# Optimization experiments

Hardware: AMD Instinct MI355X
Metric: run time of the kernel (lower is better)

The kernel has to match this reference:

```python
import math
import jax, jax.numpy as jnp
from jax import lax
import numpy as np

N, C, H, W = 32, 256, 56, 56

def setup_inputs() -> dict:
    key = jax.random.key(0)
    k = jax.random.split(key, 5)
    return {
        "x": jax.random.normal(k[0], (N, C, H, W), dtype=jnp.float32),
        "p1_w": jax.random.normal(k[1], (H, W, C, 1), dtype=jnp.float32) * 0.1,
        "conv_w": jax.random.normal(k[2], (C, C // 2, 3, 3), dtype=jnp.float32) * 0.05,
        "p4_w": jax.random.normal(k[3], (1, C, C), dtype=jnp.float32) * 0.1,
        "p5_w": jax.random.normal(k[4], (C, 1), dtype=jnp.float32) * 0.1,
    }

def reference(x, p1_w, conv_w, p4_w, p5_w):
    n, c, h, w = x.shape
    inv_sqrt_c = 1.0 / math.sqrt(c)
    # t_1: einsum 'abcd,cdef->abef' -> [n, c, c, 1] -> [n, c, c]
    t1 = jnp.einsum('nchw,hwef->ncef', x, p1_w)[..., 0]
    # t_3: grouped 3x3 conv, groups=2, no bias -> [n, c, h, w]
    t3 = lax.conv_general_dilated(
        x, conv_w, window_strides=(1, 1), padding=((1, 1), (1, 1)),
        dimension_numbers=('NCHW', 'OIHW', 'NCHW'), feature_group_count=2)
    # t_4: broadcast elementwise scale [1,c,c] * [n,c,c]
    t4 = p4_w * t1
    # t_5: [n,c,c] @ [c,1] -> [n,c]
    t5 = jnp.einsum('nab,bo->nao', t4, p5_w)[..., 0]
    # t_6: bmm(t4 [n,c,c], t3 [n,c,hw]) / sqrt(c) -> [n,c,h,w]
    t6 = (jnp.einsum('nab,nbs->nas', t4, t3.reshape(n, c, h * w))
          .reshape(n, c, h, w)) * inv_sqrt_c
    # t_7: bmm(t5 [n,1,c], x [n,c,hw]) / sqrt(c) -> [n,h,w]
    t7 = (jnp.einsum('nc,ncs->ns', t5, x.reshape(n, c, h * w))
          .reshape(n, h, w)) * inv_sqrt_c
    # t_8: broadcast add [n,1,h,w] + [n,c,h,w]
    return t7[:, None, :, :] + t6
```

## Files before the change

### kernel.cpp

```cpp
#include <hip/hip_runtime.h>

#define HWB   3136
#define HWPAD 3200
#define SPAD  3364

typedef __attribute__((ext_vector_type(8))) short bf16x8;
typedef __attribute__((ext_vector_type(4))) float f32x4;

__device__ __forceinline__ unsigned short f2bf(float f) {
    unsigned u = __float_as_uint(f);
    unsigned r = (u + 0x7fffu + ((u >> 16) & 1u)) >> 16;
    return (unsigned short)r;
}
__device__ __forceinline__ float bf2f(unsigned short h) {
    return __uint_as_float(((unsigned)h) << 16);
}
__device__ __forceinline__ void gl_lds16(const void* g, void* l) {
    __builtin_amdgcn_global_load_lds(
        (const __attribute__((address_space(1))) void*)g,
        (__attribute__((address_space(3))) void*)l, 16, 0, 0);
}

__global__ __launch_bounds__(256) void k_prep(
    const float* __restrict__ x, unsigned short* __restrict__ xc,
    unsigned short* __restrict__ xp)
{
    __shared__ short tile[64 * 66];
    const int n = blockIdx.z, c0 = blockIdx.y * 64, s0 = blockIdx.x * 64;
    const int t = threadIdx.x;
    const int cl = t >> 2;
    const int sq = (t & 3) * 16;

    const float* src = x + ((size_t)(n * 256 + c0 + cl)) * HWB + s0 + sq;
    unsigned short bf[16];
#pragma unroll
    for (int j = 0; j < 4; ++j) {
        float4 v = *(const float4*)(src + j * 4);
        bf[j * 4 + 0] = f2bf(v.x); bf[j * 4 + 1] = f2bf(v.y);
        bf[j * 4 + 2] = f2bf(v.z); bf[j * 4 + 3] = f2bf(v.w);
    }
    unsigned short* xcb = xc + ((size_t)(n * 256 + c0 + cl)) * HWB + s0 + sq;
    *(bf16x8*)xcb = *(const bf16x8*)&bf[0];
    *(bf16x8*)(xcb + 8) = *(const bf16x8*)&bf[8];
#pragma unroll
    for (int k = 0; k < 16; ++k)
        tile[(sq + k) * 66 + cl] = (short)bf[k];
    __syncthreads();
    const int r = t >> 2;
    const int cq = (t & 3) * 16;
    unsigned short ob[16];
#pragma unroll
    for (int j = 0; j < 8; ++j) {
        unsigned w = *(const unsigned*)&tile[r * 66 + cq + 2 * j];
        ob[2 * j] = (unsigned short)w;
        ob[2 * j + 1] = (unsigned short)(w >> 16);
    }
    const int s = s0 + r;
    const int sp = s + 2 * (s / 56) + 59;
    unsigned short* dst = xp + ((size_t)n * SPAD + sp) * 256 + c0 + cq;
    *(bf16x8*)dst = *(const bf16x8*)&ob[0];
    *(bf16x8*)(dst + 8) = *(const bf16x8*)&ob[8];
}

__global__ __launch_bounds__(256) void k_misc(
    const float* __restrict__ p1, const float* __restrict__ cw,
    unsigned short* __restrict__ p1t, unsigned short* __restrict__ wp,
    unsigned short* __restrict__ xp)
{
    const int b = blockIdx.x, t = threadIdx.x;
    if (b < 784) {
        __shared__ unsigned short tile[32][33];
        const int h0 = (b % 98) * 32, e0 = (b / 98) * 32;
        const int lx = t & 31, ly = t >> 5;
#pragma unroll
        for (int it = 0; it < 4; ++it) {
            int lh = ly + it * 8;
            tile[lh][lx] = f2bf(p1[(size_t)(h0 + lh) * 256 + e0 + lx]);
        }
        __syncthreads();
#pragma unroll
        for (int it = 0; it < 4; ++it) {
            int le = ly + it * 8;
            p1t[(size_t)(e0 + le) * HWB + h0 + lx] = tile[lx][le];
        }
    } else if (b < 1040) {
        const int o = b - 784;
#pragma unroll
        for (int k = t; k < 1152; k += 256) {
            int tap = k >> 7, ci = k & 127;
            wp[(size_t)o * 1152 + k] = f2bf(cw[(size_t)o * 1152 + ci * 9 + tap]);
        }
    } else {
        const int bb = b - 1040;
        const int n = bb / 29, xb = bb - n * 29;
        const int idx = xb * 256 + t;
        if (idx < 228 * 32) {
            const int i = idx >> 5, ch = idx & 31;
            int sp;
            if (i < 58)       sp = i;
            else if (i < 116) sp = 3306 + (i - 58);
            else if (i < 172) sp = (i - 115) * 58;
            else              sp = (i - 171) * 58 + 57;
            bf16x8 z = {};
            *(bf16x8*)&xp[((size_t)n * SPAD + sp) * 256 + ch * 8] = z;
        }
    }
}

__global__ __launch_bounds__(256) void k_conv(
    const unsigned short* __restrict__ xp, const unsigned short* __restrict__ wp,
    unsigned short* __restrict__ t3cl)
{
    __shared__ short As[2][128 * 64];
    __shared__ short Bs[2][128 * 64];
    const int tid = threadIdx.x;
    const int orig = blockIdx.x;
    const int wgid = (orig & 7) * 200 + (orig >> 3);
    const int ng = wgid / 25;
    const int tileS = (wgid - ng * 25) * 128;
    const int n = ng >> 1, g = ng & 1;
    const int wave = tid >> 6, lane = tid & 63;
    const int wm = (wave >> 1) * 64, wn = (wave & 1) * 64;

    const int rl = tid >> 3, q = tid & 7;
    const int swq = (q ^ (rl & 7)) * 8;

    const unsigned short* xpn = xp + (size_t)n * SPAD * 256 + g * 128 + swq;
    const unsigned short* arow[4];
    const unsigned short* brow[4];
#pragma unroll
    for (int p = 0; p < 4; ++p) {
        int s = tileS + p * 32 + rl;
        int sc = s < HWB ? s : HWB - 1;
        int sp = sc + 2 * (sc / 56) + 59;
        arow[p] = xpn + (size_t)sp * 256;
        brow[p] = wp + (size_t)(g * 128 + p * 32 + rl) * 1152 + swq;
    }

    f32x4 acc[4][4] = {};
    const int frow = lane & 15, quad = lane >> 4, sw = frow & 7;
    int rofA[4], rofB[4];
#pragma unroll
    for (int i = 0; i < 4; ++i) {
        rofA[i] = (wm + i * 16 + frow) * 64;
        rofB[i] = (wn + i * 16 + frow) * 64;
    }
    const int ldst = (tid >> 3) * 64 + (tid & 7) * 8;

    {
        const int shift0 = (-59) * 256;
#pragma unroll
        for (int p = 0; p < 4; ++p) {
            gl_lds16(arow[p] + shift0, &As[0][p * 2048 + ldst]);
            gl_lds16(brow[p], &Bs[0][p * 2048 + ldst]);
        }
    }
    __syncthreads();

    int cur = 0;
#pragma unroll
    for (int t = 0; t < 18; ++t) {
        if (t < 17) {
            const int tn = t + 1;
            const int tap = tn >> 1;
            const int shift = ((tap / 3 - 1) * 58 + (tap % 3 - 1)) * 256 + (tn & 1) * 64;
#pragma unroll
            for (int p = 0; p < 4; ++p) {
                gl_lds16(arow[p] + shift, &As[cur ^ 1][p * 2048 + ldst]);
                gl_lds16(brow[p] + tn * 64, &Bs[cur ^ 1][p * 2048 + ldst]);
            }
        }
        const short* Ab = As[cur];
        const short* Bb = Bs[cur];
#pragma unroll
        for (int h = 0; h < 2; ++h) {
            bf16x8 af[4], bfr[4];
#pragma unroll
            for (int i = 0; i < 4; ++i)
                af[i] = *(const bf16x8*)&Ab[rofA[i] + ((h * 4 + quad) ^ sw) * 8];
#pragma unroll
            for (int j = 0; j < 4; ++j)
                bfr[j] = *(const bf16x8*)&Bb[rofB[j] + ((h * 4 + quad) ^ sw) * 8];
#pragma unroll
            for (int i = 0; i < 4; ++i)
#pragma unroll
                for (int j = 0; j < 4; ++j)
                    acc[i][j] = __builtin_amdgcn_mfma_f32_16x16x32_bf16(af[i], bfr[j], acc[i][j], 0, 0, 0);
        }
        __syncthreads();
        cur ^= 1;
    }
    unsigned short* ob = t3cl + (size_t)n * HWPAD * 256 + g * 128;
#pragma unroll
    for (int i = 0; i < 4; ++i)
#pragma unroll
        for (int r = 0; r < 4; ++r) {
            int s = tileS + wm + i * 16 + (lane >> 4) * 4 + r;
            int c = wn + (lane & 15);
#pragma unroll
            for (int j = 0; j < 4; ++j) {
                float v = (s < HWB) ? acc[i][j][r] : 0.f;
                ob[(size_t)s * 256 + c + j * 16] = f2bf(v);
            }
        }
}

__global__ __launch_bounds__(256) void k_gemm1(
    const unsigned short* __restrict__ xc, const unsigned short* __restrict__ p1t,
    float* __restrict__ part)
{
    __shared__ short As[2][128 * 64];
    __shared__ short Bs[2][128 * 64];
    const int tid = threadIdx.x;
    const int orig = blockIdx.x;
    const int wgid = (orig & 7) * 64 + (orig >> 3);
    const int z = wgid >> 7;
    const int rem = wgid & 127;
    const int tileM = (rem >> 1) * 128;
    const int tileN = (rem & 1) * 128;
    const int kbase = z ? (832 + (z - 1) * 768) : 0;
    const int nk = z ? 12 : 13;
    const int wave = tid >> 6, lane = tid & 63;
    const int wm = (wave >> 1) * 64, wn = (wave & 1) * 64;

    const int rl = tid >> 3, q = tid & 7;
    const int swq = (q ^ (rl & 7)) * 8;
    const unsigned short* asrc = xc + (size_t)(tileM + rl) * HWB + kbase + swq;
    const unsigned short* bsrc = p1t + (size_t)(tileN + rl) * HWB + kbase + swq;

    f32x4 acc[4][4] = {};
    const int frow = lane & 15, quad = lane >> 4, sw = frow & 7;
    const int ldst = rl * 64 + q * 8;

#pragma unroll
    for (int p = 0; p < 4; ++p) {
        gl_lds16(asrc + (size_t)(p * 32) * HWB, &As[0][p * 2048 + ldst]);
        gl_lds16(bsrc + (size_t)(p * 32) * HWB, &Bs[0][p * 2048 + ldst]);
    }
    __syncthreads();

    int cur = 0;
    for (int i2 = 0; i2 < nk; ++i2) {
        if (i2 + 1 < nk) {
            const int kn = (i2 + 1) * 64;
#pragma unroll
            for (int p = 0; p < 4; ++p) {
                gl_lds16(asrc + (size_t)(p * 32) * HWB + kn, &As[cur ^ 1][p * 2048 + ldst]);
                gl_lds16(bsrc + (size_t)(p * 32) * HWB + kn, &Bs[cur ^ 1][p * 2048 + ldst]);
            }
        }
        const short* Ab = As[cur];
        const short* Bb = Bs[cur];
#pragma unroll
        for (int h = 0; h < 2; ++h) {
            bf16x8 af[4], bfr[4];
#pragma unroll
            for (int i = 0; i < 4; ++i)
                af[i] = *(const bf16x8*)&Ab[(wm + i * 16 + frow) * 64 + ((h * 4 + quad) ^ sw) * 8];
#pragma unroll
            for (int j = 0; j < 4; ++j)
                bfr[j] = *(const bf16x8*)&Bb[(wn + j * 16 + frow) * 64 + ((h * 4 + quad) ^ sw) * 8];
#pragma unroll
            for (int i = 0; i < 4; ++i)
#pragma unroll
                for (int j = 0; j < 4; ++j)
                    acc[i][j] = __builtin_amdgcn_mfma_f32_16x16x32_bf16(af[i], bfr[j], acc[i][j], 0, 0, 0);
        }
        __syncthreads();
        cur ^= 1;
    }
    float* ob = part + (size_t)z * 8192 * 256;
#pragma unroll
    for (int j = 0; j < 4; ++j) {
        const int e = tileN + wn + j * 16 + (lane & 15);
#pragma unroll
        for (int i = 0; i < 4; ++i)
#pragma unroll
            for (int r = 0; r < 4; ++r) {
                int m = tileM + wm + i * 16 + (lane >> 4) * 4 + r;
                ob[(size_t)m * 256 + e] = acc[i][j][r];
            }
    }
}

__global__ __launch_bounds__(256) void k_t4scale(
    const float* __restrict__ part, const float* __restrict__ p4,
    const float* __restrict__ p5, unsigned short* __restrict__ t4h,
    float* __restrict__ t5)
{
    const int row = blockIdx.x * 4 + (threadIdx.x >> 6);
    const int lane = threadIdx.x & 63;
    const size_t off = (size_t)row * 256 + lane * 4;
    const size_t slab = (size_t)8192 * 256;
    float4 a0 = *(const float4*)&part[off];
    float4 a1 = *(const float4*)&part[off + slab];
    float4 a2 = *(const float4*)&part[off + 2 * slab];
    float4 a3 = *(const float4*)&part[off + 3 * slab];
    float4 a;
    a.x = (a0.x + a1.x) + (a2.x + a3.x);
    a.y = (a0.y + a1.y) + (a2.y + a3.y);
    a.z = (a0.z + a1.z) + (a2.z + a3.z);
    a.w = (a0.w + a1.w) + (a2.w + a3.w);
    float4 sc = *(const float4*)&p4[(size_t)(row & 255) * 256 + lane * 4];
    float4 pv = *(const float4*)&p5[lane * 4];
    float v0 = a.x * sc.x, v1 = a.y * sc.y, v2 = a.z * sc.z, v3 = a.w * sc.w;
    ushort4 o;
    o.x = f2bf(v0); o.y = f2bf(v1); o.z = f2bf(v2); o.w = f2bf(v3);
    *(ushort4*)&t4h[(size_t)row * 256 + lane * 4] = o;
    float sum = v0 * pv.x + v1 * pv.y + v2 * pv.z + v3 * pv.w;
#pragma unroll
    for (int offd = 32; offd > 0; offd >>= 1) sum += __shfl_down(sum, offd);
    if (lane == 0) t5[row] = sum;
}

__global__ __launch_bounds__(256) void k_bmm(
    const unsigned short* __restrict__ t4h, const unsigned short* __restrict__ t3cl,
    const unsigned short* __restrict__ xp, const float* __restrict__ t5,
    float* __restrict__ out)
{
    __shared__ short As[2][128 * 64];
    __shared__ short Bs[2][128 * 64];
    __shared__ float t5s[256];
    __shared__ float t7loc[128];
    const int tid = threadIdx.x;
    const int orig = blockIdx.x;
    const int wgid = (orig & 7) * 200 + (orig >> 3);
    const int n = wgid / 50;
    const int rem = wgid - n * 50;
    const int tileA = (rem / 25) * 128;
    const int tileS = (rem % 25) * 128;
    const int wave = tid >> 6, lane = tid & 63;
    const int wm = (wave >> 1) * 64, wn = (wave & 1) * 64;

    const int rl = tid >> 3, q = tid & 7;
    const int swq = (q ^ (rl & 7)) * 8;
    const unsigned short* asrc = t4h + ((size_t)n * 256 + tileA + rl) * 256 + swq;
    const unsigned short* bsrc = t3cl + ((size_t)n * HWPAD + tileS + rl) * 256 + swq;

    f32x4 acc[4][4] = {};
    const int frow = lane & 15, quad = lane >> 4, sw = frow & 7;
    const int ldst = rl * 64 + q * 8;

    t5s[tid] = t5[n * 256 + tid];
#pragma unroll
    for (int p = 0; p < 4; ++p) {
        gl_lds16(asrc + (size_t)(p * 32) * 256, &As[0][p * 2048 + ldst]);
        gl_lds16(bsrc + (size_t)(p * 32) * 256, &Bs[0][p * 2048 + ldst]);
    }
    __syncthreads();

    if (tid < 128) {
        const int s = tileS + tid;
        float accv = 0.f;
        if (s < HWB) {
            const int sp = s + 2 * (s / 56) + 59;
            const unsigned short* row = xp + ((size_t)n * SPAD + sp) * 256;
#pragma unroll
            for (int j = 0; j < 32; ++j) {
                bf16x8 v = *(const bf16x8*)(row + j * 8);
#pragma unroll
                for (int k = 0; k < 8; ++k)
                    accv += t5s[j * 8 + k] * bf2f((unsigned short)v[k]);
            }
        }
        t7loc[tid] = accv * 0.0625f;
    }

    int cur = 0;
#pragma unroll
    for (int k0 = 0; k0 < 256; k0 += 64) {
        if (k0 < 192) {
            const int kn = k0 + 64;
#pragma unroll
            for (int p = 0; p < 4; ++p) {
                gl_lds16(asrc + (size_t)(p * 32) * 256 + kn, &As[cur ^ 1][p * 2048 + ldst]);
                gl_lds16(bsrc + (size_t)(p * 32) * 256 + kn, &Bs[cur ^ 1][p * 2048 + ldst]);
            }
        }
        const short* Ab = As[cur];
        const short* Bb = Bs[cur];
#pragma unroll
        for (int h = 0; h < 2; ++h) {
            bf16x8 af[4], bfr[4];
#pragma unroll
            for (int i = 0; i < 4; ++i)
                af[i] = *(const bf16x8*)&Ab[(wm + i * 16 + frow) * 64 + ((h * 4 + quad) ^ sw) * 8];
#pragma unroll
            for (int j = 0; j < 4; ++j)
                bfr[j] = *(const bf16x8*)&Bb[(wn + j * 16 + frow) * 64 + ((h * 4 + quad) ^ sw) * 8];
#pragma unroll
            for (int i = 0; i < 4; ++i)
#pragma unroll
                for (int j = 0; j < 4; ++j)
                    acc[i][j] = __builtin_amdgcn_mfma_f32_16x16x32_bf16(af[i], bfr[j], acc[i][j], 0, 0, 0);
        }
        __syncthreads();
        cur ^= 1;
    }
    float* ob = out + (size_t)n * 256 * HWB;
#pragma unroll
    for (int j = 0; j < 4; ++j) {
        const int sLoc = wn + j * 16 + (lane & 15);
        const int s = tileS + sLoc;
        if (s >= HWB) continue;
        const float t7v = t7loc[sLoc];
#pragma unroll
        for (int i = 0; i < 4; ++i)
#pragma unroll
            for (int r = 0; r < 4; ++r) {
                int a = tileA + wm + i * 16 + (lane >> 4) * 4 + r;
                ob[(size_t)a * HWB + s] = acc[i][j][r] * 0.0625f + t7v;
            }
    }
}

extern "C" void kernel_launch(void* const* d_in, const int* in_sizes, int n_in,
                              void* d_out, int out_size, void* d_ws, size_t ws_size,
                              hipStream_t stream) {
    const float* x  = (const float*)d_in[0];
    const float* p1 = (const float*)d_in[1];
    const float* cw = (const float*)d_in[2];
    const float* p4 = (const float*)d_in[3];
    const float* p5 = (const float*)d_in[4];

    char* w = (char*)d_ws;
    unsigned short* xp    = (unsigned short*)w;  w += (size_t)32 * SPAD * 256 * 2;
    unsigned short* t3cl  = (unsigned short*)w;  w += (size_t)32 * HWPAD * 256 * 2;
    unsigned short* p1t   = (unsigned short*)w;  w += (size_t)256 * HWB * 2;
    unsigned short* wpack = (unsigned short*)w;  w += (size_t)256 * 1152 * 2;
    unsigned short* t4h   = (unsigned short*)w;  w += (size_t)8192 * 256 * 2;
    float* t5             = (float*)w;           w += (size_t)8192 * 4;

    char* o = (char*)d_out;
    unsigned short* xc = (unsigned short*)o;
    float* part        = (float*)(o + (size_t)32 * 256 * HWB * 2);
    float* out = (float*)d_out;

    k_misc    <<<dim3(1968),      256, 0, stream>>>(p1, cw, p1t, wpack, xp);
    k_prep    <<<dim3(49, 4, 32), 256, 0, stream>>>(x, xc, xp);
    k_conv    <<<dim3(1600),      256, 0, stream>>>(xp, wpack, t3cl);
    k_gemm1   <<<dim3(512),       256, 0, stream>>>(xc, p1t, part);
    k_t4scale <<<dim3(2048),      256, 0, stream>>>(part, p4, p5, t4h, t5);
    k_bmm     <<<dim3(1600),      256, 0, stream>>>(t4h, t3cl, xp, t5, out);
}
```

Before: 344.6 us.

## Merge prep/misc kernels and conv/gemm1 into combined launches, halve split-K

Folds the x-conversion/transposition into the misc prep kernel and puts the grouped conv GEMM and the t1 GEMM into a single launch that branches on block index. The aim is to cut launch count and tail idle time by letting the two independent GEMMs share the GPU concurrently. The t1 GEMM split-K drops from 4 to 2 partial slabs with longer K loops, so the reduction reads less. The prep transposition now packs two channels per 32-bit LDS word. The trade-off is longer-running gemm1 blocks that may become the tail, and fewer blocks for that GEMM.

```diff
diff --git a/kernel.cpp b/kernel.cpp
--- a/kernel.cpp
+++ b/kernel.cpp
@@ -23,54 +23,52 @@
 
 __global__ __launch_bounds__(256) void k_prep(
     const float* __restrict__ x, unsigned short* __restrict__ xc,
-    unsigned short* __restrict__ xp)
-{
-    __shared__ short tile[64 * 66];
-    const int n = blockIdx.z, c0 = blockIdx.y * 64, s0 = blockIdx.x * 64;
-    const int t = threadIdx.x;
-    const int cl = t >> 2;
-    const int sq = (t & 3) * 16;
-
-    const float* src = x + ((size_t)(n * 256 + c0 + cl)) * HWB + s0 + sq;
-    unsigned short bf[16];
-#pragma unroll
-    for (int j = 0; j < 4; ++j) {
-        float4 v = *(const float4*)(src + j * 4);
-        bf[j * 4 + 0] = f2bf(v.x); bf[j * 4 + 1] = f2bf(v.y);
-        bf[j * 4 + 2] = f2bf(v.z); bf[j * 4 + 3] = f2bf(v.w);
-    }
-    unsigned short* xcb = xc + ((size_t)(n * 256 + c0 + cl)) * HWB + s0 + sq;
-    *(bf16x8*)xcb = *(const bf16x8*)&bf[0];
-    *(bf16x8*)(xcb + 8) = *(const bf16x8*)&bf[8];
-#pragma unroll
-    for (int k = 0; k < 16; ++k)
-        tile[(sq + k) * 66 + cl] = (short)bf[k];
-    __syncthreads();
-    const int r = t >> 2;
-    const int cq = (t & 3) * 16;
-    unsigned short ob[16];
-#pragma unroll
-    for (int j = 0; j < 8; ++j) {
-        unsigned w = *(const unsigned*)&tile[r * 66 + cq + 2 * j];
-        ob[2 * j] = (unsigned short)w;
-        ob[2 * j + 1] = (unsigned short)(w >> 16);
-    }
-    const int s = s0 + r;
-    const int sp = s + 2 * (s / 56) + 59;
-    unsigned short* dst = xp + ((size_t)n * SPAD + sp) * 256 + c0 + cq;
-    *(bf16x8*)dst = *(const bf16x8*)&ob[0];
-    *(bf16x8*)(dst + 8) = *(const bf16x8*)&ob[8];
-}
-
-__global__ __launch_bounds__(256) void k_misc(
+    unsigned short* __restrict__ xp,
     const float* __restrict__ p1, const float* __restrict__ cw,
-    unsigned short* __restrict__ p1t, unsigned short* __restrict__ wp,
-    unsigned short* __restrict__ xp)
+    unsigned short* __restrict__ p1t, unsigned short* __restrict__ wp)
 {
     const int b = blockIdx.x, t = threadIdx.x;
-    if (b < 784) {
+    if (b < 6272) {
+        __shared__ unsigned tile[64 * 33];
+        const int n = b / 196, rem = b - n * 196;
+        const int c0 = (rem / 49) * 64, s0 = (rem % 49) * 64;
+        const int cp = t >> 3;
+        const int sg = (t & 7) * 8;
+
+        const float* src = x + ((size_t)(n * 256 + c0 + 2 * cp)) * HWB + s0 + sg;
+        unsigned short b0[8], b1[8];
+        {
+            float4 v0 = *(const float4*)(src);
+            float4 v1 = *(const float4*)(src + 4);
+            float4 w0 = *(const float4*)(src + HWB);
+            float4 w1 = *(const float4*)(src + HWB + 4);
+            b0[0] = f2bf(v0.x); b0[1] = f2bf(v0.y); b0[2] = f2bf(v0.z); b0[3] = f2bf(v0.w);
+            b0[4] = f2bf(v1.x); b0[5] = f2bf(v1.y); b0[6] = f2bf(v1.z); b0[7] = f2bf(v1.w);
+            b1[0] = f2bf(w0.x); b1[1] = f2bf(w0.y); b1[2] = f2bf(w0.z); b1[3] = f2bf(w0.w);
+            b1[4] = f2bf(w1.x); b1[5] = f2bf(w1.y); b1[6] = f2bf(w1.z); b1[7] = f2bf(w1.w);
+        }
+        unsigned short* xcb = xc + ((size_t)(n * 256 + c0 + 2 * cp)) * HWB + s0 + sg;
+        *(bf16x8*)xcb = *(const bf16x8*)&b0[0];
+        *(bf16x8*)(xcb + HWB) = *(const bf16x8*)&b1[0];
+#pragma unroll
+        for (int k = 0; k < 8; ++k)
+            tile[(sg + k) * 33 + cp] = (unsigned)b0[k] | ((unsigned)b1[k] << 16);
+        __syncthreads();
+        const int r = t >> 2;
+        const int cq = (t & 3) * 8;
+        unsigned d[8];
+#pragma unroll
+        for (int j = 0; j < 8; ++j)
+            d[j] = tile[r * 33 + cq + j];
+        const int s = s0 + r;
+        const int sp = s + 2 * (s / 56) + 59;
+        unsigned* dst = (unsigned*)(xp + ((size_t)n * SPAD + sp) * 256 + c0 + 2 * cq);
+        *(uint4*)dst = make_uint4(d[0], d[1], d[2], d[3]);
+        *(uint4*)(dst + 4) = make_uint4(d[4], d[5], d[6], d[7]);
+    } else if (b < 7056) {
         __shared__ unsigned short tile[32][33];
-        const int h0 = (b % 98) * 32, e0 = (b / 98) * 32;
+        const int b2 = b - 6272;
+        const int h0 = (b2 % 98) * 32, e0 = (b2 / 98) * 32;
         const int lx = t & 31, ly = t >> 5;
 #pragma unroll
         for (int it = 0; it < 4; ++it) {
@@ -83,15 +81,15 @@
             int le = ly + it * 8;
             p1t[(size_t)(e0 + le) * HWB + h0 + lx] = tile[lx][le];
         }
-    } else if (b < 1040) {
-        const int o = b - 784;
+    } else if (b < 7312) {
+        const int o = b - 7056;
 #pragma unroll
         for (int k = t; k < 1152; k += 256) {
             int tap = k >> 7, ci = k & 127;
             wp[(size_t)o * 1152 + k] = f2bf(cw[(size_t)o * 1152 + ci * 9 + tap]);
         }
     } else {
-        const int bb = b - 1040;
+        const int bb = b - 7312;
         const int n = bb / 29, xb = bb - n * 29;
         const int idx = xb * 256 + t;
         if (idx < 228 * 32) {
@@ -107,179 +105,167 @@
     }
 }
 
-__global__ __launch_bounds__(256) void k_conv(
+__global__ __launch_bounds__(256) void k_mfma(
     const unsigned short* __restrict__ xp, const unsigned short* __restrict__ wp,
-    unsigned short* __restrict__ t3cl)
-{
-    __shared__ short As[2][128 * 64];
-    __shared__ short Bs[2][128 * 64];
-    const int tid = threadIdx.x;
-    const int orig = blockIdx.x;
-    const int wgid = (orig & 7) * 200 + (orig >> 3);
-    const int ng = wgid / 25;
-    const int tileS = (wgid - ng * 25) * 128;
-    const int n = ng >> 1, g = ng & 1;
-    const int wave = tid >> 6, lane = tid & 63;
-    const int wm = (wave >> 1) * 64, wn = (wave & 1) * 64;
-
-    const int rl = tid >> 3, q = tid & 7;
-    const int swq = (q ^ (rl & 7)) * 8;
-
-    const unsigned short* xpn = xp + (size_t)n * SPAD * 256 + g * 128 + swq;
-    const unsigned short* arow[4];
-    const unsigned short* brow[4];
-#pragma unroll
-    for (int p = 0; p < 4; ++p) {
-        int s = tileS + p * 32 + rl;
-        int sc = s < HWB ? s : HWB - 1;
-        int sp = sc + 2 * (sc / 56) + 59;
-        arow[p] = xpn + (size_t)sp * 256;
-        brow[p] = wp + (size_t)(g * 128 + p * 32 + rl) * 1152 + swq;
-    }
-
-    f32x4 acc[4][4] = {};
-    const int frow = lane & 15, quad = lane >> 4, sw = frow & 7;
-    int rofA[4], rofB[4];
-#pragma unroll
-    for (int i = 0; i < 4; ++i) {
-        rofA[i] = (wm + i * 16 + frow) * 64;
-        rofB[i] = (wn + i * 16 + frow) * 64;
-    }
-    const int ldst = (tid >> 3) * 64 + (tid & 7) * 8;
-
-    {
-        const int shift0 = (-59) * 256;
-#pragma unroll
-        for (int p = 0; p < 4; ++p) {
-            gl_lds16(arow[p] + shift0, &As[0][p * 2048 + ldst]);
-            gl_lds16(brow[p], &Bs[0][p * 2048 + ldst]);
-        }
-    }
-    __syncthreads();
-
-    int cur = 0;
-#pragma unroll
-    for (int t = 0; t < 18; ++t) {
-        if (t < 17) {
-            const int tn = t + 1;
-            const int tap = tn >> 1;
-            const int shift = ((tap / 3 - 1) * 58 + (tap % 3 - 1)) * 256 + (tn & 1) * 64;
-#pragma unroll
-            for (int p = 0; p < 4; ++p) {
-                gl_lds16(arow[p] + shift, &As[cur ^ 1][p * 2048 + ldst]);
-                gl_lds16(brow[p] + tn * 64, &Bs[cur ^ 1][p * 2048 + ldst]);
-            }
-        }
-        const short* Ab = As[cur];
-        const short* Bb = Bs[cur];
-#pragma unroll
-        for (int h = 0; h < 2; ++h) {
-            bf16x8 af[4], bfr[4];
-#pragma unroll
-            for (int i = 0; i < 4; ++i)
-                af[i] = *(const bf16x8*)&Ab[rofA[i] + ((h * 4 + quad) ^ sw) * 8];
-#pragma unroll
-            for (int j = 0; j < 4; ++j)
-                bfr[j] = *(const bf16x8*)&Bb[rofB[j] + ((h * 4 + quad) ^ sw) * 8];
-#pragma unroll
-            for (int i = 0; i < 4; ++i)
-#pragma unroll
-                for (int j = 0; j < 4; ++j)
-                    acc[i][j] = __builtin_amdgcn_mfma_f32_16x16x32_bf16(af[i], bfr[j], acc[i][j], 0, 0, 0);
-        }
-        __syncthreads();
-        cur ^= 1;
-    }
-    unsigned short* ob = t3cl + (size_t)n * HWPAD * 256 + g * 128;
-#pragma unroll
-    for (int i = 0; i < 4; ++i)
-#pragma unroll
-        for (int r = 0; r < 4; ++r) {
-            int s = tileS + wm + i * 16 + (lane >> 4) * 4 + r;
-            int c = wn + (lane & 15);
-#pragma unroll
-            for (int j = 0; j < 4; ++j) {
-                float v = (s < HWB) ? acc[i][j][r] : 0.f;
-                ob[(size_t)s * 256 + c + j * 16] = f2bf(v);
-            }
-        }
-}
-
-__global__ __launch_bounds__(256) void k_gemm1(
+    unsigned short* __restrict__ t3cl,
     const unsigned short* __restrict__ xc, const unsigned short* __restrict__ p1t,
     float* __restrict__ part)
 {
     __shared__ short As[2][128 * 64];
     __shared__ short Bs[2][128 * 64];
     const int tid = threadIdx.x;
-    const int orig = blockIdx.x;
-    const int wgid = (orig & 7) * 64 + (orig >> 3);
-    const int z = wgid >> 7;
-    const int rem = wgid & 127;
-    const int tileM = (rem >> 1) * 128;
-    const int tileN = (rem & 1) * 128;
-    const int kbase = z ? (832 + (z - 1) * 768) : 0;
-    const int nk = z ? 12 : 13;
     const int wave = tid >> 6, lane = tid & 63;
     const int wm = (wave >> 1) * 64, wn = (wave & 1) * 64;
-
     const int rl = tid >> 3, q = tid & 7;
     const int swq = (q ^ (rl & 7)) * 8;
-    const unsigned short* asrc = xc + (size_t)(tileM + rl) * HWB + kbase + swq;
-    const unsigned short* bsrc = p1t + (size_t)(tileN + rl) * HWB + kbase + swq;
-
-    f32x4 acc[4][4] = {};
+    const int ldst = rl * 64 + q * 8;
     const int frow = lane & 15, quad = lane >> 4, sw = frow & 7;
-    const int ldst = rl * 64 + q * 8;
-
-#pragma unroll
-    for (int p = 0; p < 4; ++p) {
-        gl_lds16(asrc + (size_t)(p * 32) * HWB, &As[0][p * 2048 + ldst]);
-        gl_lds16(bsrc + (size_t)(p * 32) * HWB, &Bs[0][p * 2048 + ldst]);
-    }
-    __syncthreads();
-
-    int cur = 0;
-    for (int i2 = 0; i2 < nk; ++i2) {
-        if (i2 + 1 < nk) {
-            const int kn = (i2 + 1) * 64;
+
+    if (blockIdx.x < 1600) {
+        const int orig = blockIdx.x;
+        const int wgid = (orig & 7) * 200 + (orig >> 3);
+        const int ng = wgid / 25;
+        const int tileS = (wgid - ng * 25) * 128;
+        const int n = ng >> 1, g = ng & 1;
+
+        const unsigned short* xpn = xp + (size_t)n * SPAD * 256 + g * 128 + swq;
+        const unsigned short* arow[4];
+        const unsigned short* brow[4];
+#pragma unroll
+        for (int p = 0; p < 4; ++p) {
+            int s = tileS + p * 32 + rl;
+            int sc = s < HWB ? s : HWB - 1;
+            int sp = sc + 2 * (sc / 56) + 59;
+            arow[p] = xpn + (size_t)sp * 256;
+            brow[p] = wp + (size_t)(g * 128 + p * 32 + rl) * 1152 + swq;
+        }
+
+        f32x4 acc[4][4] = {};
+        int rofA[4], rofB[4];
+#pragma unroll
+        for (int i = 0; i < 4; ++i) {
+            rofA[i] = (wm + i * 16 + frow) * 64;
+            rofB[i] = (wn + i * 16 + frow) * 64;
+        }
+        {
+            const int shift0 = (-59) * 256;
 #pragma unroll
             for (int p = 0; p < 4; ++p) {
-                gl_lds16(asrc + (size_t)(p * 32) * HWB + kn, &As[cur ^ 1][p * 2048 + ldst]);
-                gl_lds16(bsrc + (size_t)(p * 32) * HWB + kn, &Bs[cur ^ 1][p * 2048 + ldst]);
-            }
-        }
-        const short* Ab = As[cur];
-        const short* Bb = Bs[cur];
-#pragma unroll
-        for (int h = 0; h < 2; ++h) {
-            bf16x8 af[4], bfr[4];
+                gl_lds16(arow[p] + shift0, &As[0][p * 2048 + ldst]);
+                gl_lds16(brow[p], &Bs[0][p * 2048 + ldst]);
+            }
+        }
+        __syncthreads();
+
+        int cur = 0;
+#pragma unroll
+        for (int t = 0; t < 18; ++t) {
+            if (t < 17) {
+                const int tn = t + 1;
+                const int tap = tn >> 1;
+                const int shift = ((tap / 3 - 1) * 58 + (tap % 3 - 1)) * 256 + (tn & 1) * 64;
+#pragma unroll
+                for (int p = 0; p < 4; ++p) {
+                    gl_lds16(arow[p] + shift, &As[cur ^ 1][p * 2048 + ldst]);
+                    gl_lds16(brow[p] + tn * 64, &Bs[cur ^ 1][p * 2048 + ldst]);
+                }
+            }
+            const short* Ab = As[cur];
+            const short* Bb = Bs[cur];
+#pragma unroll
+            for (int h = 0; h < 2; ++h) {
+                bf16x8 af[4], bfr[4];
+#pragma unroll
+                for (int i = 0; i < 4; ++i)
+                    af[i] = *(const bf16x8*)&Ab[rofA[i] + ((h * 4 + quad) ^ sw) * 8];
+#pragma unroll
+                for (int j = 0; j < 4; ++j)
+                    bfr[j] = *(const bf16x8*)&Bb[rofB[j] + ((h * 4 + quad) ^ sw) * 8];
+#pragma unroll
+                for (int i = 0; i < 4; ++i)
+#pragma unroll
+                    for (int j = 0; j < 4; ++j)
+                        acc[i][j] = __builtin_amdgcn_mfma_f32_16x16x32_bf16(af[i], bfr[j], acc[i][j], 0, 0, 0);
+            }
+            __syncthreads();
+            cur ^= 1;
+        }
+        unsigned short* ob = t3cl + (size_t)n * HWPAD * 256 + g * 128;
+#pragma unroll
+        for (int i = 0; i < 4; ++i)
+#pragma unroll
+            for (int r = 0; r < 4; ++r) {
+                int s = tileS + wm + i * 16 + quad * 4 + r;
+                int c = wn + frow;
+#pragma unroll
+                for (int j = 0; j < 4; ++j) {
+                    float v = (s < HWB) ? acc[i][j][r] : 0.f;
+                    ob[(size_t)s * 256 + c + j * 16] = f2bf(v);
+                }
+            }
+    } else {
+        const int orig = blockIdx.x - 1600;
+        const int wgid = (orig & 7) * 32 + (orig >> 3);
+        const int z = wgid >> 7;
+        const int rem = wgid & 127;
+        const int tileM = (rem >> 1) * 128;
+        const int tileN = (rem & 1) * 128;
+        const int kbase = z * 1600;
+        const int nk = z ? 24 : 25;
+
+        const unsigned short* asrc = xc + (size_t)(tileM + rl) * HWB + kbase + swq;
+        const unsigned short* bsrc = p1t + (size_t)(tileN + rl) * HWB + kbase + swq;
+
+        f32x4 acc[4][4] = {};
+#pragma unroll
+        for (int p = 0; p < 4; ++p) {
+            gl_lds16(asrc + (size_t)(p * 32) * HWB, &As[0][p * 2048 + ldst]);
+            gl_lds16(bsrc + (size_t)(p * 32) * HWB, &Bs[0][p * 2048 + ldst]);
+        }
+        __syncthreads();
+
+        int cur = 0;
+        for (int i2 = 0; i2 < nk; ++i2) {
+            if (i2 + 1 < nk) {
+                const int kn = (i2 + 1) * 64;
+#pragma unroll
+                for (int p = 0; p < 4; ++p) {
+                    gl_lds16(asrc + (size_t)(p * 32) * HWB + kn, &As[cur ^ 1][p * 2048 + ldst]);
+                    gl_lds16(bsrc + (size_t)(p * 32) * HWB + kn, &Bs[cur ^ 1][p * 2048 + ldst]);
+                }
+            }
+            const short* Ab = As[cur];
+            const short* Bb = Bs[cur];
+#pragma unroll
+            for (int h = 0; h < 2; ++h) {
+                bf16x8 af[4], bfr[4];
+#pragma unroll
+                for (int i = 0; i < 4; ++i)
+                    af[i] = *(const bf16x8*)&Ab[(wm + i * 16 + frow) * 64 + ((h * 4 + quad) ^ sw) * 8];
+#pragma unroll
+                for (int j = 0; j < 4; ++j)
+                    bfr[j] = *(const bf16x8*)&Bb[(wn + j * 16 + frow) * 64 + ((h * 4 + quad) ^ sw) * 8];
+#pragma unroll
+                for (int i = 0; i < 4; ++i)
+#pragma unroll
+                    for (int j = 0; j < 4; ++j)
+                        acc[i][j] = __builtin_amdgcn_mfma_f32_16x16x32_bf16(af[i], bfr[j], acc[i][j], 0, 0, 0);
+            }
+            __syncthreads();
+            cur ^= 1;
+        }
+        float* ob = part + (size_t)z * 8192 * 256;
+#pragma unroll
+        for (int j = 0; j < 4; ++j) {
+            const int e = tileN + wn + j * 16 + frow;
 #pragma unroll
             for (int i = 0; i < 4; ++i)
-                af[i] = *(const bf16x8*)&Ab[(wm + i * 16 + frow) * 64 + ((h * 4 + quad) ^ sw) * 8];
-#pragma unroll
-            for (int j = 0; j < 4; ++j)
-                bfr[j] = *(const bf16x8*)&Bb[(wn + j * 16 + frow) * 64 + ((h * 4 + quad) ^ sw) * 8];
-#pragma unroll
-            for (int i = 0; i < 4; ++i)
-#pragma unroll
-                for (int j = 0; j < 4; ++j)
-                    acc[i][j] = __builtin_amdgcn_mfma_f32_16x16x32_bf16(af[i], bfr[j], acc[i][j], 0, 0, 0);
-        }
-        __syncthreads();
-        cur ^= 1;
-    }
-    float* ob = part + (size_t)z * 8192 * 256;
-#pragma unroll
-    for (int j = 0; j < 4; ++j) {
-        const int e = tileN + wn + j * 16 + (lane & 15);
-#pragma unroll
-        for (int i = 0; i < 4; ++i)
-#pragma unroll
-            for (int r = 0; r < 4; ++r) {
-                int m = tileM + wm + i * 16 + (lane >> 4) * 4 + r;
-                ob[(size_t)m * 256 + e] = acc[i][j][r];
-            }
+#pragma unroll
+                for (int r = 0; r < 4; ++r) {
+                    int m = tileM + wm + i * 16 + quad * 4 + r;
+                    ob[(size_t)m * 256 + e] = acc[i][j][r];
+                }
+        }
     }
 }
 
@@ -294,13 +280,8 @@
     const size_t slab = (size_t)8192 * 256;
     float4 a0 = *(const float4*)&part[off];
     float4 a1 = *(const float4*)&part[off + slab];
-    float4 a2 = *(const float4*)&part[off + 2 * slab];
-    float4 a3 = *(const float4*)&part[off + 3 * slab];
     float4 a;
-    a.x = (a0.x + a1.x) + (a2.x + a3.x);
-    a.y = (a0.y + a1.y) + (a2.y + a3.y);
-    a.z = (a0.z + a1.z) + (a2.z + a3.z);
-    a.w = (a0.w + a1.w) + (a2.w + a3.w);
+    a.x = a0.x + a1.x; a.y = a0.y + a1.y; a.z = a0.z + a1.z; a.w = a0.w + a1.w;
     float4 sc = *(const float4*)&p4[(size_t)(row & 255) * 256 + lane * 4];
     float4 pv = *(const float4*)&p5[lane * 4];
     float v0 = a.x * sc.x, v1 = a.y * sc.y, v2 = a.z * sc.z, v3 = a.w * sc.w;
@@ -400,7 +381,7 @@
     float* ob = out + (size_t)n * 256 * HWB;
 #pragma unroll
     for (int j = 0; j < 4; ++j) {
-        const int sLoc = wn + j * 16 + (lane & 15);
+        const int sLoc = wn + j * 16 + frow;
         const int s = tileS + sLoc;
         if (s >= HWB) continue;
         const float t7v = t7loc[sLoc];
@@ -408,7 +389,7 @@
         for (int i = 0; i < 4; ++i)
 #pragma unroll
             for (int r = 0; r < 4; ++r) {
-                int a = tileA + wm + i * 16 + (lane >> 4) * 4 + r;
+                int a = tileA + wm + i * 16 + quad * 4 + r;
                 ob[(size_t)a * HWB + s] = acc[i][j][r] * 0.0625f + t7v;
             }
     }
@@ -436,10 +417,8 @@
     float* part        = (float*)(o + (size_t)32 * 256 * HWB * 2);
     float* out = (float*)d_out;
 
-    k_misc    <<<dim3(1968),      256, 0, stream>>>(p1, cw, p1t, wpack, xp);
-    k_prep    <<<dim3(49, 4, 32), 256, 0, stream>>>(x, xc, xp);
-    k_conv    <<<dim3(1600),      256, 0, stream>>>(xp, wpack, t3cl);
-    k_gemm1   <<<dim3(512),       256, 0, stream>>>(xc, p1t, part);
-    k_t4scale <<<dim3(2048),      256, 0, stream>>>(part, p4, p5, t4h, t5);
-    k_bmm     <<<dim3(1600),      256, 0, stream>>>(t4h, t3cl, xp, t5, out);
-}
+    k_prep    <<<dim3(8240),  256, 0, stream>>>(x, xc, xp, p1, cw, p1t, wpack);
+    k_mfma    <<<dim3(1856),  256, 0, stream>>>(xp, wpack, t3cl, xc, p1t, part);
+    k_t4scale <<<dim3(2048),  256, 0, stream>>>(part, p4, p5, t4h, t5);
+    k_bmm     <<<dim3(1600),  256, 0, stream>>>(t4h, t3cl, xp, t5, out);
+}
```

Result: faster. 329.9 us (-4.3%).
